# Kernel tuning notes

Hardware: AMD Instinct MI355X
Metric: run time of the kernel (lower is better)

## Reference

```python
import jax, jax.numpy as jnp
import numpy as np

B, T, H = 8, 2048, 1024
P = 64           # num_attention_project
N = 4096         # config.n (bias table length), N >= 2T-1
WINDOW = 64      # relative_attention
NEG = -10000.0


def setup_inputs() -> dict:
    key = jax.random.key(0)
    ks = jax.random.split(key, 10)
    s = 1.0 / np.sqrt(H)
    sp = 1.0 / np.sqrt(P)
    sb = 1.0 / np.sqrt(N)
    return {
        "attn_input": jax.random.normal(ks[0], (B, T, H), dtype=jnp.float32),
        "attention_mask": jnp.ones((B, T), dtype=jnp.float32),
        # Linear weights stored as [in, out] so y = x @ W + b
        "Wq": jax.random.uniform(ks[1], (H, P), minval=-s, maxval=s),
        "bq": jnp.zeros((P,), jnp.float32),
        "Wk": jax.random.uniform(ks[2], (H, P), minval=-s, maxval=s),
        "bk": jnp.zeros((P,), jnp.float32),
        "Wv": jax.random.uniform(ks[3], (H, P), minval=-s, maxval=s),
        "bv": jnp.zeros((P,), jnp.float32),
        "Wo": jax.random.uniform(ks[4], (P, H), minval=-sp, maxval=sp),
        "bo": jnp.zeros((H,), jnp.float32),
        "bias": jax.random.uniform(ks[5], (N,), minval=-sb, maxval=sb),
    }


def reference(attn_input, attention_mask, Wq, bq, Wk, bk, Wv, bv, Wo, bo, bias):
    q = attn_input @ Wq + bq            # [B,T,P]
    k = attn_input @ Wk + bk
    v = attn_input @ Wv + bv
    scores = jnp.einsum("btp,bsp->bts", q, k) / jnp.sqrt(jnp.float32(P))  # [B,T,T]
    # padding mask: note original broadcasts over COLUMNS via unsqueeze(-1)
    scores = scores + (1.0 - attention_mask)[:, :, None] * NEG
    # circulant window mask: keep |i-j| <= WINDOW (all ones if WINDOW >= T)
    i = jnp.arange(T)
    rel = i[:, None] - i[None, :]       # i - j
    win = (jnp.abs(rel) <= WINDOW) | (WINDOW >= T)
    scores = scores + jnp.where(win, 0.0, NEG)[None, :, :]
    # gathered learnable relative-position bias: bias[n//2 - i + j]
    scores = scores + bias[N // 2 - rel][None, :, :]
    attn = jax.nn.softmax(scores, axis=-1)
    out = jnp.einsum("bts,bsp->btp", attn, v)
    return out @ Wo + bo                # [B,T,H]
```

## Files before the change

### kernel.cpp

```cpp
#include <hip/hip_runtime.h>

using bf16x8 = __attribute__((ext_vector_type(8))) short;
using f32x4  = __attribute__((ext_vector_type(4))) float;

static __device__ inline unsigned short f2bf(float f) {
  unsigned int u = __float_as_uint(f);
  u += 0x7fffu + ((u >> 16) & 1u);
  return (unsigned short)(u >> 16);
}
static __device__ inline unsigned int pk2(float a, float b) {
  return (unsigned int)f2bf(a) | ((unsigned int)f2bf(b) << 16);
}

#define ROW16_MAX(x) { \
  { int _t = __builtin_amdgcn_update_dpp(0, __float_as_int(x), 0x121, 0xf, 0xf, true); x = fmaxf(x, __int_as_float(_t)); } \
  { int _t = __builtin_amdgcn_update_dpp(0, __float_as_int(x), 0x122, 0xf, 0xf, true); x = fmaxf(x, __int_as_float(_t)); } \
  { int _t = __builtin_amdgcn_update_dpp(0, __float_as_int(x), 0x124, 0xf, 0xf, true); x = fmaxf(x, __int_as_float(_t)); } \
  { int _t = __builtin_amdgcn_update_dpp(0, __float_as_int(x), 0x128, 0xf, 0xf, true); x = fmaxf(x, __int_as_float(_t)); } }
#define ROW16_SUM(x) { \
  { int _t = __builtin_amdgcn_update_dpp(0, __float_as_int(x), 0x121, 0xf, 0xf, true); x += __int_as_float(_t); } \
  { int _t = __builtin_amdgcn_update_dpp(0, __float_as_int(x), 0x122, 0xf, 0xf, true); x += __int_as_float(_t); } \
  { int _t = __builtin_amdgcn_update_dpp(0, __float_as_int(x), 0x124, 0xf, 0xf, true); x += __int_as_float(_t); } \
  { int _t = __builtin_amdgcn_update_dpp(0, __float_as_int(x), 0x128, 0xf, 0xf, true); x += __int_as_float(_t); } }

__global__ __launch_bounds__(256) void prep_kernel(
    const float* __restrict__ Wq, const float* __restrict__ Wk, const float* __restrict__ Wv,
    const float* __restrict__ Wo, const float* __restrict__ bq, const float* __restrict__ bk,
    const float* __restrict__ bv,
    unsigned short* __restrict__ Wt, unsigned short* __restrict__ Wot, float* __restrict__ bqkv)
{
  int idx = blockIdx.x * 256 + threadIdx.x;
  if (idx < 192 * 1024) {
    int n = idx >> 10, k = idx & 1023;
    const float* W = (n < 64) ? Wq : (n < 128) ? Wk : Wv;
    Wt[idx] = f2bf(W[k * 64 + (n & 63)]);
  } else if (idx < 192 * 1024 + 1024 * 64) {
    int j = idx - 192 * 1024;
    int n = j >> 6, k = j & 63;
    Wot[j] = f2bf(Wo[k * 1024 + n]);
  } else if (idx < 192 * 1024 + 1024 * 64 + 192) {
    int n = idx - (192 * 1024 + 1024 * 64);
    bqkv[n] = (n < 64) ? bq[n] : (n < 128) ? bk[n - 64] : bv[n - 128];
  }
}

__global__ __launch_bounds__(256) void qkv_gemm(
    const float* __restrict__ X, const unsigned short* __restrict__ Wt,
    const float* __restrict__ bqkv, float* __restrict__ qkv)
{
  __shared__ __align__(16) unsigned short As[32 * 72];
  __shared__ __align__(16) unsigned short Bs[96 * 72];
  int t = threadIdx.x;
  int lane = t & 63, w = t >> 6;
  int m0 = (blockIdx.x >> 1) * 32;
  int nbase = (blockIdx.x & 1) * 96;
  int mg = w & 1, ng = w >> 1;
  int col = lane & 15, quad = lane >> 4;
  f32x4 acc[3] = {};

  int rowA = t >> 3, cA = t & 7;
  const float* srcA = X + (size_t)(m0 + rowA) * 1024 + cA * 8;
  const unsigned short* srcB = Wt + (size_t)(nbase + rowA) * 1024 + cA * 8;

  for (int ks = 0; ks < 16; ++ks) {
    __syncthreads();
    {
      const float* s = srcA + ks * 64;
      float4 f0 = *(const float4*)(s);
      float4 f1 = *(const float4*)(s + 4);
      uint4 p;
      p.x = pk2(f0.x, f0.y); p.y = pk2(f0.z, f0.w);
      p.z = pk2(f1.x, f1.y); p.w = pk2(f1.z, f1.w);
      *(uint4*)(As + rowA * 72 + cA * 8) = p;
    }
    #pragma unroll
    for (int r = 0; r < 3; ++r) {
      *(uint4*)(Bs + (rowA + 32 * r) * 72 + cA * 8) =
          *(const uint4*)(srcB + (size_t)(32 * r) * 1024 + ks * 64);
    }
    __syncthreads();
    #pragma unroll
    for (int kk = 0; kk < 64; kk += 32) {
      int ko = kk + quad * 8;
      bf16x8 a = *(const bf16x8*)(As + (mg * 16 + col) * 72 + ko);
      #pragma unroll
      for (int ns = 0; ns < 3; ++ns) {
        bf16x8 b = *(const bf16x8*)(Bs + ((ng * 3 + ns) * 16 + col) * 72 + ko);
        acc[ns] = __builtin_amdgcn_mfma_f32_16x16x32_bf16(a, b, acc[ns], 0, 0, 0);
      }
    }
  }
  #pragma unroll
  for (int ns = 0; ns < 3; ++ns)
    #pragma unroll
    for (int r = 0; r < 4; ++r) {
      int m = m0 + mg * 16 + quad * 4 + r;
      int n = nbase + ng * 48 + ns * 16 + col;
      qkv[(size_t)m * 192 + n] = acc[ns][r] + bqkv[n];
    }
}

__global__ __launch_bounds__(256) void band_attn(
    const float* __restrict__ qkv, const float* __restrict__ bias,
    unsigned short* __restrict__ attnout)
{
  __shared__ __align__(16) unsigned short Kl[192 * 72];
  __shared__ __align__(16) unsigned short Vt[64 * 216];
  __shared__ __align__(16) unsigned short Ps[4 * 16 * 168];
  __shared__ float biasL[129];

  int t = threadIdx.x;
  int lane = t & 63, w = t >> 6;
  int col = lane & 15, quad = lane >> 4;
  int bidx = blockIdx.x;
  int b = bidx >> 5;
  int i0 = (bidx & 31) * 64;
  int jw = i0 - 64;
  const float* qbase = qkv + (size_t)(b << 11) * 192;

  if (t < 129) biasL[t] = bias[1984 + t];
  #pragma unroll
  for (int it = 0; it < 24; ++it) {
    int row = it * 8 + (t >> 5);
    int colq = (t & 31) * 4;
    int jb = jw + row;
    int jc = jb < 0 ? 0 : (jb > 2047 ? 2047 : jb);
    const float* src = qbase + (size_t)jc * 192 + 64 + colq;
    float4 f = *(const float4*)src;
    if (colq < 64) {
      *(uint2*)(Kl + row * 72 + colq) = make_uint2(pk2(f.x, f.y), pk2(f.z, f.w));
    } else {
      int p0 = colq - 64;
      Vt[(p0 + 0) * 216 + row] = f2bf(f.x);
      Vt[(p0 + 1) * 216 + row] = f2bf(f.y);
      Vt[(p0 + 2) * 216 + row] = f2bf(f.z);
      Vt[(p0 + 3) * 216 + row] = f2bf(f.w);
    }
  }
  {
    int p = t >> 2, c0 = 192 + (t & 3) * 4;
    *(uint2*)(Vt + p * 216 + c0) = make_uint2(0u, 0u);
  }
  __syncthreads();

  int iq = i0 + w * 16;
  bf16x8 aq0, aq1;
  {
    const float* qr = qbase + (size_t)(iq + col) * 192 + quad * 8;
    float4 f0 = *(const float4*)(qr);
    float4 f1 = *(const float4*)(qr + 4);
    float4 f2 = *(const float4*)(qr + 32);
    float4 f3 = *(const float4*)(qr + 36);
    union { bf16x8 v; uint4 u; } c0_, c1_;
    c0_.u = make_uint4(pk2(f0.x, f0.y), pk2(f0.z, f0.w), pk2(f1.x, f1.y), pk2(f1.z, f1.w));
    c1_.u = make_uint4(pk2(f2.x, f2.y), pk2(f2.z, f2.w), pk2(f3.x, f3.y), pk2(f3.z, f3.w));
    aq0 = c0_.v; aq1 = c1_.v;
  }
  f32x4 s[9];
  #pragma unroll
  for (int t9 = 0; t9 < 9; ++t9) {
    int krow = ((w + t9) * 16 + col) * 72;
    bf16x8 kb0 = *(const bf16x8*)(Kl + krow + quad * 8);
    bf16x8 kb1 = *(const bf16x8*)(Kl + krow + 32 + quad * 8);
    f32x4 z = {};
    z = __builtin_amdgcn_mfma_f32_16x16x32_bf16(aq0, kb0, z, 0, 0, 0);
    s[t9] = __builtin_amdgcn_mfma_f32_16x16x32_bf16(aq1, kb1, z, 0, 0, 0);
  }
  int q4 = quad * 4;
  float mrow[4] = {-3e38f, -3e38f, -3e38f, -3e38f};
  #pragma unroll
  for (int t9 = 0; t9 < 9; ++t9) {
    int j = iq - 64 + t9 * 16 + col;
    #pragma unroll
    for (int r = 0; r < 4; ++r) {
      int diff = q4 + r + 64 - t9 * 16 - col;
      bool valid = (j >= 0) & (j < 2048) & (diff >= -64) & (diff <= 64);
      int bi = 64 - diff; bi = bi < 0 ? 0 : (bi > 128 ? 128 : bi);
      float sv = valid ? (s[t9][r] * 0.125f + biasL[bi]) : -3e38f;
      s[t9][r] = sv;
      mrow[r] = fmaxf(mrow[r], sv);
    }
  }
  #pragma unroll
  for (int r = 0; r < 4; ++r) ROW16_MAX(mrow[r]);
  unsigned short* Pw = Ps + w * (16 * 168);
  float lsum[4] = {0.f, 0.f, 0.f, 0.f};
  #pragma unroll
  for (int t9 = 0; t9 < 9; ++t9)
    #pragma unroll
    for (int r = 0; r < 4; ++r) {
      float p = __expf(s[t9][r] - mrow[r]);
      lsum[r] += p;
      Pw[(q4 + r) * 168 + t9 * 16 + col] = f2bf(p);
    }
  #pragma unroll
  for (int r = 0; r < 4; ++r) {
    ROW16_SUM(lsum[r]);
    Pw[(q4 + r) * 168 + 144 + col] = 0;
  }
  f32x4 o[4] = {};
  #pragma unroll
  for (int kc = 0; kc < 5; ++kc) {
    bf16x8 pa = *(const bf16x8*)(Pw + col * 168 + kc * 32 + quad * 8);
    #pragma unroll
    for (int nt = 0; nt < 4; ++nt) {
      bf16x8 vb = *(const bf16x8*)(Vt + (nt * 16 + col) * 216 + 16 * w + kc * 32 + quad * 8);
      o[nt] = __builtin_amdgcn_mfma_f32_16x16x32_bf16(pa, vb, o[nt], 0, 0, 0);
    }
  }
  float rl[4];
  #pragma unroll
  for (int r = 0; r < 4; ++r) rl[r] = 1.0f / lsum[r];
  #pragma unroll
  for (int nt = 0; nt < 4; ++nt)
    #pragma unroll
    for (int r = 0; r < 4; ++r) {
      int arow = (b << 11) + iq + q4 + r;
      attnout[(size_t)arow * 64 + nt * 16 + col] = f2bf(o[nt][r] * rl[r]);
    }
}

__global__ __launch_bounds__(256) void out_gemm(
    const unsigned short* __restrict__ attn, const unsigned short* __restrict__ Wot,
    const float* __restrict__ bo, float* __restrict__ out)
{
  __shared__ __align__(16) unsigned short As[64 * 72];
  __shared__ __align__(16) unsigned short Bs[128 * 72];
  int t = threadIdx.x, lane = t & 63, w = t >> 6;
  int m0 = (blockIdx.x >> 3) * 64;
  int n0 = (blockIdx.x & 7) * 128;
  #pragma unroll
  for (int r = 0; r < 2; ++r) {
    int tau = t + 256 * r; int row = tau >> 3, c = tau & 7;
    *(uint4*)(As + row * 72 + c * 8) =
        *(const uint4*)(attn + (size_t)(m0 + row) * 64 + c * 8);
  }
  #pragma unroll
  for (int r = 0; r < 4; ++r) {
    int tau = t + 256 * r; int n = tau >> 3, c = tau & 7;
    *(uint4*)(Bs + n * 72 + c * 8) =
        *(const uint4*)(Wot + (size_t)(n0 + n) * 64 + c * 8);
  }
  __syncthreads();
  f32x4 acc[2][4] = {};
  int mg = w & 1, ngg = w >> 1;
  #pragma unroll
  for (int kk = 0; kk < 64; kk += 32) {
    int ko = kk + (lane >> 4) * 8;
    bf16x8 a0 = *(const bf16x8*)(As + (mg * 32 +      (lane & 15)) * 72 + ko);
    bf16x8 a1 = *(const bf16x8*)(As + (mg * 32 + 16 + (lane & 15)) * 72 + ko);
    #pragma unroll
    for (int ns = 0; ns < 4; ++ns) {
      bf16x8 b = *(const bf16x8*)(Bs + ((ngg * 4 + ns) * 16 + (lane & 15)) * 72 + ko);
      acc[0][ns] = __builtin_amdgcn_mfma_f32_16x16x32_bf16(a0, b, acc[0][ns], 0, 0, 0);
      acc[1][ns] = __builtin_amdgcn_mfma_f32_16x16x32_bf16(a1, b, acc[1][ns], 0, 0, 0);
    }
  }
  int col = lane & 15, q = lane >> 4;
  #pragma unroll
  for (int ms = 0; ms < 2; ++ms)
    #pragma unroll
    for (int ns = 0; ns < 4; ++ns)
      #pragma unroll
      for (int r = 0; r < 4; ++r) {
        int mm = m0 + mg * 32 + ms * 16 + q * 4 + r;
        int nn = n0 + (ngg * 4 + ns) * 16 + col;
        out[(size_t)mm * 1024 + nn] = acc[ms][ns][r] + bo[nn];
      }
}

extern "C" void kernel_launch(void* const* d_in, const int* in_sizes, int n_in,
                              void* d_out, int out_size, void* d_ws, size_t ws_size,
                              hipStream_t stream) {
  const float* X    = (const float*)d_in[0];
  const float* Wq   = (const float*)d_in[2];
  const float* bq   = (const float*)d_in[3];
  const float* Wk   = (const float*)d_in[4];
  const float* bk   = (const float*)d_in[5];
  const float* Wv   = (const float*)d_in[6];
  const float* bv   = (const float*)d_in[7];
  const float* Wo   = (const float*)d_in[8];
  const float* bo   = (const float*)d_in[9];
  const float* bias = (const float*)d_in[10];
  float* out = (float*)d_out;
  char* ws = (char*)d_ws;
  float*          qkv  = (float*)(ws);
  unsigned short* attn = (unsigned short*)(ws + 12582912);
  unsigned short* Wt   = (unsigned short*)(ws + 14680064);
  unsigned short* Wot  = (unsigned short*)(ws + 15073280);
  float*          bqkv = (float*)(ws + 15204352);

  prep_kernel<<<1025, 256, 0, stream>>>(Wq, Wk, Wv, Wo, bq, bk, bv, Wt, Wot, bqkv);
  qkv_gemm<<<1024, 256, 0, stream>>>(X, Wt, bqkv, qkv);
  band_attn<<<256, 256, 0, stream>>>(qkv, bias, attn);
  out_gemm<<<2048, 256, 0, stream>>>(attn, Wot, bo, out);
}
```

Measured before the change: 178.5 us.

## Store QKV intermediate as bf16 and double-buffer qkv_gemm shared tiles

The QKV projection now writes its result as bf16 instead of fp32. This halves the intermediate's memory traffic and lets band_attn load K, V and Q directly, with no in-kernel conversion. qkv_gemm also gains double-buffered LDS tiles with register prefetch of the next k-slice, which overlaps global loads with MFMA work and removes one barrier per iteration. Rounding QKV to bf16 earlier adds a little precision loss, though band_attn already converted to bf16 before.

```diff
diff --git a/kernel.cpp b/kernel.cpp
--- a/kernel.cpp
+++ b/kernel.cpp
@@ -46,10 +46,10 @@
 
 __global__ __launch_bounds__(256) void qkv_gemm(
     const float* __restrict__ X, const unsigned short* __restrict__ Wt,
-    const float* __restrict__ bqkv, float* __restrict__ qkv)
-{
-  __shared__ __align__(16) unsigned short As[32 * 72];
-  __shared__ __align__(16) unsigned short Bs[96 * 72];
+    const float* __restrict__ bqkv, unsigned short* __restrict__ qkvb)
+{
+  __shared__ __align__(16) unsigned short As[2][32 * 72];
+  __shared__ __align__(16) unsigned short Bs[2][96 * 72];
   int t = threadIdx.x;
   int lane = t & 63, w = t >> 6;
   int m0 = (blockIdx.x >> 1) * 32;
@@ -62,30 +62,40 @@
   const float* srcA = X + (size_t)(m0 + rowA) * 1024 + cA * 8;
   const unsigned short* srcB = Wt + (size_t)(nbase + rowA) * 1024 + cA * 8;
 
+  float4 f0 = *(const float4*)(srcA);
+  float4 f1 = *(const float4*)(srcA + 4);
+  uint4 b0 = *(const uint4*)(srcB);
+  uint4 b1 = *(const uint4*)(srcB + 32 * 1024);
+  uint4 b2 = *(const uint4*)(srcB + 64 * 1024);
+
   for (int ks = 0; ks < 16; ++ks) {
-    __syncthreads();
+    int cur = ks & 1;
     {
-      const float* s = srcA + ks * 64;
-      float4 f0 = *(const float4*)(s);
-      float4 f1 = *(const float4*)(s + 4);
       uint4 p;
       p.x = pk2(f0.x, f0.y); p.y = pk2(f0.z, f0.w);
       p.z = pk2(f1.x, f1.y); p.w = pk2(f1.z, f1.w);
-      *(uint4*)(As + rowA * 72 + cA * 8) = p;
-    }
-    #pragma unroll
-    for (int r = 0; r < 3; ++r) {
-      *(uint4*)(Bs + (rowA + 32 * r) * 72 + cA * 8) =
-          *(const uint4*)(srcB + (size_t)(32 * r) * 1024 + ks * 64);
+      *(uint4*)(As[cur] + rowA * 72 + cA * 8) = p;
+      *(uint4*)(Bs[cur] + rowA * 72 + cA * 8) = b0;
+      *(uint4*)(Bs[cur] + (rowA + 32) * 72 + cA * 8) = b1;
+      *(uint4*)(Bs[cur] + (rowA + 64) * 72 + cA * 8) = b2;
+    }
+    if (ks < 15) {
+      const float* sA = srcA + (ks + 1) * 64;
+      f0 = *(const float4*)(sA);
+      f1 = *(const float4*)(sA + 4);
+      const unsigned short* sB = srcB + (ks + 1) * 64;
+      b0 = *(const uint4*)(sB);
+      b1 = *(const uint4*)(sB + 32 * 1024);
+      b2 = *(const uint4*)(sB + 64 * 1024);
     }
     __syncthreads();
     #pragma unroll
     for (int kk = 0; kk < 64; kk += 32) {
       int ko = kk + quad * 8;
-      bf16x8 a = *(const bf16x8*)(As + (mg * 16 + col) * 72 + ko);
+      bf16x8 a = *(const bf16x8*)(As[cur] + (mg * 16 + col) * 72 + ko);
       #pragma unroll
       for (int ns = 0; ns < 3; ++ns) {
-        bf16x8 b = *(const bf16x8*)(Bs + ((ng * 3 + ns) * 16 + col) * 72 + ko);
+        bf16x8 b = *(const bf16x8*)(Bs[cur] + ((ng * 3 + ns) * 16 + col) * 72 + ko);
         acc[ns] = __builtin_amdgcn_mfma_f32_16x16x32_bf16(a, b, acc[ns], 0, 0, 0);
       }
     }
@@ -96,12 +106,12 @@
     for (int r = 0; r < 4; ++r) {
       int m = m0 + mg * 16 + quad * 4 + r;
       int n = nbase + ng * 48 + ns * 16 + col;
-      qkv[(size_t)m * 192 + n] = acc[ns][r] + bqkv[n];
+      qkvb[(size_t)m * 192 + n] = f2bf(acc[ns][r] + bqkv[n]);
     }
 }
 
 __global__ __launch_bounds__(256) void band_attn(
-    const float* __restrict__ qkv, const float* __restrict__ bias,
+    const unsigned short* __restrict__ qkvb, const float* __restrict__ bias,
     unsigned short* __restrict__ attnout)
 {
   __shared__ __align__(16) unsigned short Kl[192 * 72];
@@ -116,25 +126,30 @@
   int b = bidx >> 5;
   int i0 = (bidx & 31) * 64;
   int jw = i0 - 64;
-  const float* qbase = qkv + (size_t)(b << 11) * 192;
+  const unsigned short* qbase = qkvb + (size_t)(b << 11) * 192;
+
+  int iq = i0 + w * 16;
+  const unsigned short* qr = qbase + (size_t)(iq + col) * 192 + quad * 8;
+  bf16x8 aq0 = *(const bf16x8*)(qr);
+  bf16x8 aq1 = *(const bf16x8*)(qr + 32);
 
   if (t < 129) biasL[t] = bias[1984 + t];
   #pragma unroll
-  for (int it = 0; it < 24; ++it) {
-    int row = it * 8 + (t >> 5);
-    int colq = (t & 31) * 4;
+  for (int it = 0; it < 12; ++it) {
+    int idx = it * 256 + t;
+    int row = idx >> 4;
+    int c = idx & 15;
     int jb = jw + row;
     int jc = jb < 0 ? 0 : (jb > 2047 ? 2047 : jb);
-    const float* src = qbase + (size_t)jc * 192 + 64 + colq;
-    float4 f = *(const float4*)src;
-    if (colq < 64) {
-      *(uint2*)(Kl + row * 72 + colq) = make_uint2(pk2(f.x, f.y), pk2(f.z, f.w));
+    const unsigned short* src = qbase + (size_t)jc * 192 + 64 + c * 8;
+    uint4 v = *(const uint4*)src;
+    if (c < 8) {
+      *(uint4*)(Kl + row * 72 + c * 8) = v;
     } else {
-      int p0 = colq - 64;
-      Vt[(p0 + 0) * 216 + row] = f2bf(f.x);
-      Vt[(p0 + 1) * 216 + row] = f2bf(f.y);
-      Vt[(p0 + 2) * 216 + row] = f2bf(f.z);
-      Vt[(p0 + 3) * 216 + row] = f2bf(f.w);
+      union { uint4 u; unsigned short s[8]; } uv; uv.u = v;
+      int p0 = (c - 8) * 8;
+      #pragma unroll
+      for (int e = 0; e < 8; ++e) Vt[(p0 + e) * 216 + row] = uv.s[e];
     }
   }
   {
@@ -143,19 +158,6 @@
   }
   __syncthreads();
 
-  int iq = i0 + w * 16;
-  bf16x8 aq0, aq1;
-  {
-    const float* qr = qbase + (size_t)(iq + col) * 192 + quad * 8;
-    float4 f0 = *(const float4*)(qr);
-    float4 f1 = *(const float4*)(qr + 4);
-    float4 f2 = *(const float4*)(qr + 32);
-    float4 f3 = *(const float4*)(qr + 36);
-    union { bf16x8 v; uint4 u; } c0_, c1_;
-    c0_.u = make_uint4(pk2(f0.x, f0.y), pk2(f0.z, f0.w), pk2(f1.x, f1.y), pk2(f1.z, f1.w));
-    c1_.u = make_uint4(pk2(f2.x, f2.y), pk2(f2.z, f2.w), pk2(f3.x, f3.y), pk2(f3.z, f3.w));
-    aq0 = c0_.v; aq1 = c1_.v;
-  }
   f32x4 s[9];
   #pragma unroll
   for (int t9 = 0; t9 < 9; ++t9) {
@@ -284,14 +286,14 @@
   const float* bias = (const float*)d_in[10];
   float* out = (float*)d_out;
   char* ws = (char*)d_ws;
-  float*          qkv  = (float*)(ws);
-  unsigned short* attn = (unsigned short*)(ws + 12582912);
-  unsigned short* Wt   = (unsigned short*)(ws + 14680064);
-  unsigned short* Wot  = (unsigned short*)(ws + 15073280);
-  float*          bqkv = (float*)(ws + 15204352);
+  unsigned short* qkvb = (unsigned short*)(ws);
+  unsigned short* attn = (unsigned short*)(ws + 6291456);
+  unsigned short* Wt   = (unsigned short*)(ws + 8388608);
+  unsigned short* Wot  = (unsigned short*)(ws + 8781824);
+  float*          bqkv = (float*)(ws + 8912896);
 
   prep_kernel<<<1025, 256, 0, stream>>>(Wq, Wk, Wv, Wo, bq, bk, bv, Wt, Wot, bqkv);
-  qkv_gemm<<<1024, 256, 0, stream>>>(X, Wt, bqkv, qkv);
-  band_attn<<<256, 256, 0, stream>>>(qkv, bias, attn);
+  qkv_gemm<<<1024, 256, 0, stream>>>(X, Wt, bqkv, qkvb);
+  band_attn<<<256, 256, 0, stream>>>(qkvb, bias, attn);
   out_gemm<<<2048, 256, 0, stream>>>(attn, Wot, bo, out);
 }
```

New measurement: 167.7 us. -6.0%, faster.
